# Optimization experiments

Hardware: AMD Instinct MI355X
Metric: run time of the kernel (lower is better)

## Reference

```python
import jax, jax.numpy as jnp
import numpy as np

K = 5  # Chebyshev order


def laplacian(w):
    # normalized Laplacian: I - D^{-1/2} W D^{-1/2}
    d = jnp.sum(w, axis=1)
    d_re = 1.0 / jnp.sqrt(d + 1e-5)
    return jnp.eye(w.shape[0], dtype=w.dtype) - d_re[:, None] * w * d_re[None, :]


def cheb_terms(x, lap, k):
    # x: [B,N,C], lap: [N,N] -> [B,k,N,C]
    # Faithful to torch code: T0 = ones, then (x, lap@x) recurrence for k>2.
    t0 = jnp.ones_like(x)
    if k == 1:
        return t0[:, None]
    t1 = jnp.matmul(lap, x)
    if k == 2:
        return jnp.stack([t0, t1], axis=1)
    terms = [t0, x, t1]
    tkm1, tk = x, t1
    for _ in range(3, k):
        tkm1, tk = tk, 2.0 * jnp.matmul(lap, tk) - tkm1
        terms.append(tk)
    return jnp.stack(terms, axis=1)


def graph_conv(x, lap, w, k):
    # torch: cp.permute(0,2,3,1).flatten(2) @ w, i.e. flat index = c*k + t
    t = cheb_terms(x, lap, k)                       # [B,k,N,C]
    C = x.shape[-1]
    O = w.shape[-1]
    return jnp.einsum('bknc,cko->bno', t, w.reshape(C, k, O))


def setup_inputs() -> dict:
    key = jax.random.key(0)
    ks = jax.random.split(key, 9)
    B, N, Cin, H = 8192, 32, 60, 128
    return {
        'x': jax.random.normal(ks[0], (B, N, Cin), dtype=jnp.float32),
        'adj': jax.random.normal(ks[1], (N, N), dtype=jnp.float32) * 0.1,
        'adj_bias': jax.random.normal(ks[2], (1,), dtype=jnp.float32) * 0.1 + 0.2,
        'w1': jax.random.normal(ks[3], (K * Cin, H), dtype=jnp.float32) * 0.05,
        'b1': jax.random.normal(ks[4], (1, 1, H), dtype=jnp.float32) * 0.05,
        'w2': jax.random.normal(ks[5], (K * H, H), dtype=jnp.float32) * 0.05,
        'b2': jax.random.normal(ks[6], (1, 1, H), dtype=jnp.float32) * 0.05,
        'fc_w': jax.random.normal(ks[7], (2, N * H), dtype=jnp.float32) * 0.02,
        'fc_b': jax.random.normal(ks[8], (2,), dtype=jnp.float32) * 0.02,
    }


def reference(x, adj, adj_bias, w1, b1, w2, b2, fc_w, fc_b):
    # DGCNN.forward (eval mode: dropout = identity)
    a = jax.nn.relu(adj + adj_bias)
    lap = laplacian(a)
    h = graph_conv(x, lap, w1, K)
    h = jax.nn.relu(h + b1)      # B1ReLU
    h = graph_conv(h, lap, w2, K)
    h = jax.nn.relu(h + b2)
    h = h.reshape(h.shape[0], -1)  # [B, N*H]
    return h @ fc_w.T + fc_b
```

## Files before the change

### kernel.cpp

```cpp
#include <hip/hip_runtime.h>

typedef unsigned short u16;
typedef unsigned int u32;
typedef short bf16x8 __attribute__((ext_vector_type(8)));
typedef float f32x4 __attribute__((ext_vector_type(4)));

#define MFMA16(a, b, c) __builtin_amdgcn_mfma_f32_16x16x32_bf16((a), (b), (c), 0, 0, 0)

__device__ __forceinline__ u16 f2bf(float f) {
  u32 u = __builtin_bit_cast(u32, f);
  u += 0x7FFFu + ((u >> 16) & 1u);
  return (u16)(u >> 16);
}
__device__ __forceinline__ u32 pk2bf(float a, float b) {
#if __has_builtin(__builtin_amdgcn_cvt_pk_bf16_f32)
  auto v = __builtin_amdgcn_cvt_pk_bf16_f32(a, b);
  return __builtin_bit_cast(u32, v);
#else
  return (u32)f2bf(a) | ((u32)f2bf(b) << 16);
#endif
}

#define WS_MGF   0
#define WS_WT1F  8192
#define WS_WT2F  73728
#define WS_B1    204800
#define WS_B2    205312

__global__ void prep_kernel(const float* __restrict__ adj,
                            const float* __restrict__ adj_bias,
                            const float* __restrict__ w1,
                            const float* __restrict__ b1,
                            const float* __restrict__ w2,
                            const float* __restrict__ b2,
                            char* __restrict__ ws) {
  const int tid = threadIdx.x;
  if (blockIdx.x == 0) {
    __shared__ float sa[1024], Ls[1024], L2s[1024], L3s[1024], sdre[32];
    float bias = adj_bias[0];
    for (int i = tid; i < 1024; i += 256) sa[i] = fmaxf(adj[i] + bias, 0.0f);
    __syncthreads();
    if (tid < 32) {
      float s = 0.0f;
      for (int c = 0; c < 32; ++c) s += sa[tid * 32 + c];
      sdre[tid] = 1.0f / sqrtf(s + 1e-5f);
    }
    __syncthreads();
    for (int i = tid; i < 1024; i += 256) {
      int n = i >> 5, c = i & 31;
      Ls[i] = (n == c ? 1.0f : 0.0f) - sdre[n] * sa[i] * sdre[c];
    }
    __syncthreads();
    for (int i = tid; i < 1024; i += 256) {
      int r = i >> 5, c = i & 31;
      float s = 0.0f;
      for (int m = 0; m < 32; ++m) s += Ls[r * 32 + m] * Ls[m * 32 + c];
      L2s[i] = s;
    }
    __syncthreads();
    for (int i = tid; i < 1024; i += 256) {
      int r = i >> 5, c = i & 31;
      float s = 0.0f;
      for (int m = 0; m < 32; ++m) s += L2s[r * 32 + m] * Ls[m * 32 + c];
      L3s[i] = s;
    }
    __syncthreads();
    u16* MGf = (u16*)(ws + WS_MGF);
    for (int i = tid; i < 4096; i += 256) {
      int jt = i >> 9, lane = (i >> 3) & 63, j = i & 7;
      int col = jt * 16 + (lane & 15);
      int k = ((lane >> 4) << 3) + j;
      int kk = col >> 5, np = col & 31;
      float v;
      if (kk == 0)      v = (np == k) ? 1.0f : 0.0f;
      else if (kk == 1) v = Ls[np * 32 + k];
      else if (kk == 2) v = 2.0f * L2s[np * 32 + k] - (np == k ? 1.0f : 0.0f);
      else              v = 4.0f * L3s[np * 32 + k] - 3.0f * Ls[np * 32 + k];
      MGf[i] = f2bf(v);
    }
    float* B1 = (float*)(ws + WS_B1);
    float* B2 = (float*)(ws + WS_B2);
    if (tid < 128) {
      float s = b1[tid];
      for (int c = 0; c < 60; ++c) s += w1[(c * 5) * 128 + tid];
      B1[tid] = s;
    } else {
      int o = tid - 128;
      float s = b2[o];
      for (int c = 0; c < 128; ++c) s += w2[(c * 5) * 128 + o];
      B2[o] = s;
    }
  } else {
    u16* WT1F = (u16*)(ws + WS_WT1F);
    u16* WT2F = (u16*)(ws + WS_WT2F);
    int g = (blockIdx.x - 1) * 256 + tid;
    for (int i = g; i < 32768; i += 16 * 256) {
      int j = i & 7, lane = (i >> 3) & 63, ks = (i >> 9) & 3;
      int h = (i >> 11) & 1, ot = i >> 12;
      int q = lane >> 4;
      int c = h * 32 + q * 8 + j;
      int o = ot * 16 + (lane & 15);
      WT1F[i] = (c < 60) ? f2bf(w1[(c * 5 + ks + 1) * 128 + o]) : (u16)0;
    }
    for (int i = g; i < 65536; i += 16 * 256) {
      int j = i & 7, lane = (i >> 3) & 63, ks = (i >> 9) & 3;
      int h = (i >> 11) & 3, mt = i >> 13;
      int q = lane >> 4;
      int c2 = h * 32 + q * 8 + j;
      int o = mt * 16 + (lane & 15);
      WT2F[i] = f2bf(w2[(c2 * 5 + ks + 1) * 128 + o]);
    }
  }
}

__global__ __launch_bounds__(256, 4) void dgcnn_kernel(
    const float* __restrict__ x,
    const char* __restrict__ ws,
    const float* __restrict__ fc_w,
    const float* __restrict__ fc_b,
    float* __restrict__ out) {
  __shared__ __align__(16) char arena[35840];
  __shared__ float red[16];
  u16* XtA = (u16*)arena;
  u16* XtB = (u16*)(arena + 5120);
  u16* HtA = (u16*)arena;
  u16* HtB = (u16*)(arena + 9216);
  u16* YA  = (u16*)(arena + 18432);
  u16* YB  = (u16*)(arena + 27136);

  const u16* MGf  = (const u16*)(ws + WS_MGF);
  const u16* WT1F = (const u16*)(ws + WS_WT1F);
  const u16* WT2F = (const u16*)(ws + WS_WT2F);
  const float* bias1 = (const float*)(ws + WS_B1);
  const float* bias2 = (const float*)(ws + WS_B2);

  const int tid = threadIdx.x;
  const int w = tid >> 6, lane = tid & 63;
  const int l15 = lane & 15, q = lane >> 4;
  const int b0 = blockIdx.x * 2;
  const f32x4 z4 = {0.0f, 0.0f, 0.0f, 0.0f};

  bf16x8 mB0 = *(const bf16x8*)(MGf + ((2 * w + 0) * 64 + lane) * 8);
  bf16x8 mB1 = *(const bf16x8*)(MGf + ((2 * w + 1) * 64 + lane) * 8);

  for (int i = tid; i < 160; i += 256) {
    int r = 60 + i / 40, c = i % 40;
    XtA[r * 40 + c] = 0;
    XtB[r * 40 + c] = 0;
  }
  const float* xb = x + (size_t)b0 * 1920;
  for (int i = tid; i < 1920; i += 256) {
    int n = i / 60, c = i - n * 60;
    u32 p = pk2bf(xb[i], xb[1920 + i]);
    XtA[c * 40 + n] = (u16)p;
    XtB[c * 40 + n] = (u16)(p >> 16);
  }
  __syncthreads();

  f32x4 acc1A[2][2] = {{z4, z4}, {z4, z4}};
  f32x4 acc1B[2][2] = {{z4, z4}, {z4, z4}};
#pragma unroll
  for (int h = 0; h < 2; ++h) {
    {
      f32x4 gA[2][2], gB[2][2];
#pragma unroll
      for (int mtl = 0; mtl < 2; ++mtl) {
        int roff = ((2 * h + mtl) * 16 + l15) * 40 + q * 8;
        bf16x8 aA = *(const bf16x8*)&XtA[roff];
        bf16x8 aB = *(const bf16x8*)&XtB[roff];
        gA[mtl][0] = MFMA16(aA, mB0, z4);
        gA[mtl][1] = MFMA16(aA, mB1, z4);
        gB[mtl][0] = MFMA16(aB, mB0, z4);
        gB[mtl][1] = MFMA16(aB, mB1, z4);
      }
#pragma unroll
      for (int mtl = 0; mtl < 2; ++mtl)
#pragma unroll
        for (int jtl = 0; jtl < 2; ++jtl) {
          int np = jtl * 16 + l15;
          int off = np * 136 + w * 32 + mtl * 16 + q * 4;
          uint2 vA, vB;
          vA.x = pk2bf(gA[mtl][jtl][0], gA[mtl][jtl][1]);
          vA.y = pk2bf(gA[mtl][jtl][2], gA[mtl][jtl][3]);
          vB.x = pk2bf(gB[mtl][jtl][0], gB[mtl][jtl][1]);
          vB.y = pk2bf(gB[mtl][jtl][2], gB[mtl][jtl][3]);
          *(uint2*)&YA[off] = vA;
          *(uint2*)&YB[off] = vB;
        }
    }
    __syncthreads();
#pragma unroll
    for (int ks = 0; ks < 4; ++ks) {
      bf16x8 wfa = *(const bf16x8*)(WT1F + ((((2 * w + 0) * 2 + h) * 4 + ks) * 64 + lane) * 8);
      bf16x8 wfb = *(const bf16x8*)(WT1F + ((((2 * w + 1) * 2 + h) * 4 + ks) * 64 + lane) * 8);
      int yoff = ks * 32 + q * 8;
      bf16x8 a0A = *(const bf16x8*)&YA[l15 * 136 + yoff];
      bf16x8 a1A = *(const bf16x8*)&YA[(16 + l15) * 136 + yoff];
      bf16x8 a0B = *(const bf16x8*)&YB[l15 * 136 + yoff];
      bf16x8 a1B = *(const bf16x8*)&YB[(16 + l15) * 136 + yoff];
      acc1A[0][0] = MFMA16(a0A, wfa, acc1A[0][0]);
      acc1A[0][1] = MFMA16(a0A, wfb, acc1A[0][1]);
      acc1A[1][0] = MFMA16(a1A, wfa, acc1A[1][0]);
      acc1A[1][1] = MFMA16(a1A, wfb, acc1A[1][1]);
      acc1B[0][0] = MFMA16(a0B, wfa, acc1B[0][0]);
      acc1B[0][1] = MFMA16(a0B, wfb, acc1B[0][1]);
      acc1B[1][0] = MFMA16(a1B, wfa, acc1B[1][0]);
      acc1B[1][1] = MFMA16(a1B, wfb, acc1B[1][1]);
    }
    if (h == 0) __syncthreads();
  }
#pragma unroll
  for (int ot = 0; ot < 2; ++ot) {
    int o = (2 * w + ot) * 16 + l15;
    float bv = bias1[o];
#pragma unroll
    for (int mt = 0; mt < 2; ++mt) {
      int off = o * 36 + mt * 16 + q * 4;
      uint2 vA, vB;
      vA.x = pk2bf(fmaxf(acc1A[mt][ot][0] + bv, 0.0f), fmaxf(acc1A[mt][ot][1] + bv, 0.0f));
      vA.y = pk2bf(fmaxf(acc1A[mt][ot][2] + bv, 0.0f), fmaxf(acc1A[mt][ot][3] + bv, 0.0f));
      vB.x = pk2bf(fmaxf(acc1B[mt][ot][0] + bv, 0.0f), fmaxf(acc1B[mt][ot][1] + bv, 0.0f));
      vB.y = pk2bf(fmaxf(acc1B[mt][ot][2] + bv, 0.0f), fmaxf(acc1B[mt][ot][3] + bv, 0.0f));
      *(uint2*)&HtA[off] = vA;
      *(uint2*)&HtB[off] = vB;
    }
  }
  __syncthreads();

  f32x4 acc2A[2][2] = {{z4, z4}, {z4, z4}};
  f32x4 acc2B[2][2] = {{z4, z4}, {z4, z4}};
#pragma unroll
  for (int h = 0; h < 4; ++h) {
    {
      f32x4 gA[2][2], gB[2][2];
#pragma unroll
      for (int mtl = 0; mtl < 2; ++mtl) {
        int roff = ((2 * h + mtl) * 16 + l15) * 36 + q * 8;
        bf16x8 aA = *(const bf16x8*)&HtA[roff];
        bf16x8 aB = *(const bf16x8*)&HtB[roff];
        gA[mtl][0] = MFMA16(aA, mB0, z4);
        gA[mtl][1] = MFMA16(aA, mB1, z4);
        gB[mtl][0] = MFMA16(aB, mB0, z4);
        gB[mtl][1] = MFMA16(aB, mB1, z4);
      }
#pragma unroll
      for (int mtl = 0; mtl < 2; ++mtl)
#pragma unroll
        for (int jtl = 0; jtl < 2; ++jtl) {
          int np = jtl * 16 + l15;
          int off = np * 136 + w * 32 + mtl * 16 + q * 4;
          uint2 vA, vB;
          vA.x = pk2bf(gA[mtl][jtl][0], gA[mtl][jtl][1]);
          vA.y = pk2bf(gA[mtl][jtl][2], gA[mtl][jtl][3]);
          vB.x = pk2bf(gB[mtl][jtl][0], gB[mtl][jtl][1]);
          vB.y = pk2bf(gB[mtl][jtl][2], gB[mtl][jtl][3]);
          *(uint2*)&YA[off] = vA;
          *(uint2*)&YB[off] = vB;
        }
    }
    __syncthreads();
#pragma unroll
    for (int ks = 0; ks < 4; ++ks) {
      bf16x8 wfa = *(const bf16x8*)(WT2F + ((((2 * w + 0) * 4 + h) * 4 + ks) * 64 + lane) * 8);
      bf16x8 wfb = *(const bf16x8*)(WT2F + ((((2 * w + 1) * 4 + h) * 4 + ks) * 64 + lane) * 8);
      int yoff = ks * 32 + q * 8;
      bf16x8 by0A = *(const bf16x8*)&YA[l15 * 136 + yoff];
      bf16x8 by1A = *(const bf16x8*)&YA[(16 + l15) * 136 + yoff];
      bf16x8 by0B = *(const bf16x8*)&YB[l15 * 136 + yoff];
      bf16x8 by1B = *(const bf16x8*)&YB[(16 + l15) * 136 + yoff];
      acc2A[0][0] = MFMA16(wfa, by0A, acc2A[0][0]);
      acc2A[0][1] = MFMA16(wfa, by1A, acc2A[0][1]);
      acc2A[1][0] = MFMA16(wfb, by0A, acc2A[1][0]);
      acc2A[1][1] = MFMA16(wfb, by1A, acc2A[1][1]);
      acc2B[0][0] = MFMA16(wfa, by0B, acc2B[0][0]);
      acc2B[0][1] = MFMA16(wfa, by1B, acc2B[0][1]);
      acc2B[1][0] = MFMA16(wfb, by0B, acc2B[1][0]);
      acc2B[1][1] = MFMA16(wfb, by1B, acc2B[1][1]);
    }
    if (h < 3) __syncthreads();
  }

  float p0A = 0.0f, p1A = 0.0f, p0B = 0.0f, p1B = 0.0f;
#pragma unroll
  for (int ot = 0; ot < 2; ++ot) {
    int ob = (2 * w + ot) * 16 + q * 4;
    float4 bv = *(const float4*)&bias2[ob];
#pragma unroll
    for (int nt = 0; nt < 2; ++nt) {
      int n = nt * 16 + l15;
      float4 w0 = *(const float4*)&fc_w[n * 128 + ob];
      float4 w1v = *(const float4*)&fc_w[4096 + n * 128 + ob];
      float hA0 = fmaxf(acc2A[ot][nt][0] + bv.x, 0.0f);
      float hA1 = fmaxf(acc2A[ot][nt][1] + bv.y, 0.0f);
      float hA2 = fmaxf(acc2A[ot][nt][2] + bv.z, 0.0f);
      float hA3 = fmaxf(acc2A[ot][nt][3] + bv.w, 0.0f);
      float hB0 = fmaxf(acc2B[ot][nt][0] + bv.x, 0.0f);
      float hB1 = fmaxf(acc2B[ot][nt][1] + bv.y, 0.0f);
      float hB2 = fmaxf(acc2B[ot][nt][2] + bv.z, 0.0f);
      float hB3 = fmaxf(acc2B[ot][nt][3] + bv.w, 0.0f);
      p0A = fmaf(hA0, w0.x, fmaf(hA1, w0.y, fmaf(hA2, w0.z, fmaf(hA3, w0.w, p0A))));
      p1A = fmaf(hA0, w1v.x, fmaf(hA1, w1v.y, fmaf(hA2, w1v.z, fmaf(hA3, w1v.w, p1A))));
      p0B = fmaf(hB0, w0.x, fmaf(hB1, w0.y, fmaf(hB2, w0.z, fmaf(hB3, w0.w, p0B))));
      p1B = fmaf(hB0, w1v.x, fmaf(hB1, w1v.y, fmaf(hB2, w1v.z, fmaf(hB3, w1v.w, p1B))));
    }
  }
#pragma unroll
  for (int off = 32; off >= 1; off >>= 1) {
    p0A += __shfl_xor(p0A, off);
    p1A += __shfl_xor(p1A, off);
    p0B += __shfl_xor(p0B, off);
    p1B += __shfl_xor(p1B, off);
  }
  if (lane == 0) {
    red[w * 4 + 0] = p0A;
    red[w * 4 + 1] = p1A;
    red[w * 4 + 2] = p0B;
    red[w * 4 + 3] = p1B;
  }
  __syncthreads();
  if (tid < 4) {
    float s = red[tid] + red[4 + tid] + red[8 + tid] + red[12 + tid] + fc_b[tid & 1];
    out[(b0 + (tid >> 1)) * 2 + (tid & 1)] = s;
  }
}

extern "C" void kernel_launch(void* const* d_in, const int* in_sizes, int n_in,
                              void* d_out, int out_size, void* d_ws, size_t ws_size,
                              hipStream_t stream) {
  const float* x        = (const float*)d_in[0];
  const float* adj      = (const float*)d_in[1];
  const float* adj_bias = (const float*)d_in[2];
  const float* w1       = (const float*)d_in[3];
  const float* b1       = (const float*)d_in[4];
  const float* w2       = (const float*)d_in[5];
  const float* b2       = (const float*)d_in[6];
  const float* fc_w     = (const float*)d_in[7];
  const float* fc_b     = (const float*)d_in[8];
  float* out = (float*)d_out;
  char* ws   = (char*)d_ws;

  prep_kernel<<<17, 256, 0, stream>>>(adj, adj_bias, w1, b1, w2, b2, ws);
  dgcnn_kernel<<<4096, 256, 0, stream>>>(x, ws, fc_w, fc_b, out);
}
```

Before: 194.7 us.

## Swizzle LDS layouts, vectorize input staging, shrink shared memory for higher occupancy

```diff
diff --git a/kernel.cpp b/kernel.cpp
--- a/kernel.cpp
+++ b/kernel.cpp
@@ -4,6 +4,7 @@
 typedef unsigned int u32;
 typedef short bf16x8 __attribute__((ext_vector_type(8)));
 typedef float f32x4 __attribute__((ext_vector_type(4)));
+typedef u32 u32x4 __attribute__((ext_vector_type(4)));
 
 #define MFMA16(a, b, c) __builtin_amdgcn_mfma_f32_16x16x32_bf16((a), (b), (c), 0, 0, 0)
 
@@ -98,7 +99,7 @@
       int j = i & 7, lane = (i >> 3) & 63, ks = (i >> 9) & 3;
       int h = (i >> 11) & 1, ot = i >> 12;
       int q = lane >> 4;
-      int c = h * 32 + q * 8 + j;
+      int c = h * 32 + ((j >> 2) << 4) + q * 4 + (j & 3);
       int o = ot * 16 + (lane & 15);
       WT1F[i] = (c < 60) ? f2bf(w1[(c * 5 + ks + 1) * 128 + o]) : (u16)0;
     }
@@ -106,27 +107,27 @@
       int j = i & 7, lane = (i >> 3) & 63, ks = (i >> 9) & 3;
       int h = (i >> 11) & 3, mt = i >> 13;
       int q = lane >> 4;
-      int c2 = h * 32 + q * 8 + j;
+      int c2 = h * 32 + ((j >> 2) << 4) + q * 4 + (j & 3);
       int o = mt * 16 + (lane & 15);
       WT2F[i] = f2bf(w2[(c2 * 5 + ks + 1) * 128 + o]);
     }
   }
 }
 
-__global__ __launch_bounds__(256, 4) void dgcnn_kernel(
+__global__ __launch_bounds__(256, 5) void dgcnn_kernel(
     const float* __restrict__ x,
     const char* __restrict__ ws,
     const float* __restrict__ fc_w,
     const float* __restrict__ fc_b,
     float* __restrict__ out) {
-  __shared__ __align__(16) char arena[35840];
-  __shared__ float red[16];
+  __shared__ __align__(16) char arena[32768];
   u16* XtA = (u16*)arena;
   u16* XtB = (u16*)(arena + 5120);
   u16* HtA = (u16*)arena;
-  u16* HtB = (u16*)(arena + 9216);
-  u16* YA  = (u16*)(arena + 18432);
-  u16* YB  = (u16*)(arena + 27136);
+  u16* HtB = (u16*)(arena + 8192);
+  u16* YA  = (u16*)(arena + 16384);
+  u16* YB  = (u16*)(arena + 24576);
+  float* red = (float*)arena;
 
   const u16* MGf  = (const u16*)(ws + WS_MGF);
   const u16* WT1F = (const u16*)(ws + WS_WT1F);
@@ -143,19 +144,34 @@
   bf16x8 mB0 = *(const bf16x8*)(MGf + ((2 * w + 0) * 64 + lane) * 8);
   bf16x8 mB1 = *(const bf16x8*)(MGf + ((2 * w + 1) * 64 + lane) * 8);
 
-  for (int i = tid; i < 160; i += 256) {
-    int r = 60 + i / 40, c = i % 40;
-    XtA[r * 40 + c] = 0;
-    XtB[r * 40 + c] = 0;
-  }
   const float* xb = x + (size_t)b0 * 1920;
-  for (int i = tid; i < 1920; i += 256) {
-    int n = i / 60, c = i - n * 60;
-    u32 p = pk2bf(xb[i], xb[1920 + i]);
-    XtA[c * 40 + n] = (u16)p;
-    XtB[c * 40 + n] = (u16)(p >> 16);
+  {
+    int tn = (tid & 15) * 2;
+    int tc = (tid >> 4) * 4;
+    if (tc < 60) {
+      float4 a0 = *(const float4*)(xb + tn * 60 + tc);
+      float4 a1 = *(const float4*)(xb + tn * 60 + 60 + tc);
+      float4 c0 = *(const float4*)(xb + 1920 + tn * 60 + tc);
+      float4 c1 = *(const float4*)(xb + 1920 + tn * 60 + 60 + tc);
+      *(u32*)&XtA[(tc + 0) * 40 + tn] = pk2bf(a0.x, a1.x);
+      *(u32*)&XtA[(tc + 1) * 40 + tn] = pk2bf(a0.y, a1.y);
+      *(u32*)&XtA[(tc + 2) * 40 + tn] = pk2bf(a0.z, a1.z);
+      *(u32*)&XtA[(tc + 3) * 40 + tn] = pk2bf(a0.w, a1.w);
+      *(u32*)&XtB[(tc + 0) * 40 + tn] = pk2bf(c0.x, c1.x);
+      *(u32*)&XtB[(tc + 1) * 40 + tn] = pk2bf(c0.y, c1.y);
+      *(u32*)&XtB[(tc + 2) * 40 + tn] = pk2bf(c0.z, c1.z);
+      *(u32*)&XtB[(tc + 3) * 40 + tn] = pk2bf(c0.w, c1.w);
+    } else {
+#pragma unroll
+      for (int j = 0; j < 4; ++j) {
+        *(u32*)&XtA[(tc + j) * 40 + tn] = 0;
+        *(u32*)&XtB[(tc + j) * 40 + tn] = 0;
+      }
+    }
   }
   __syncthreads();
+
+  const int ysw_w = ((w * 4 + q) ^ (l15 & 7)) * 8;
 
   f32x4 acc1A[2][2] = {{z4, z4}, {z4, z4}};
   f32x4 acc1B[2][2] = {{z4, z4}, {z4, z4}};
@@ -174,30 +190,31 @@
         gB[mtl][1] = MFMA16(aB, mB1, z4);
       }
 #pragma unroll
-      for (int mtl = 0; mtl < 2; ++mtl)
-#pragma unroll
-        for (int jtl = 0; jtl < 2; ++jtl) {
-          int np = jtl * 16 + l15;
-          int off = np * 136 + w * 32 + mtl * 16 + q * 4;
-          uint2 vA, vB;
-          vA.x = pk2bf(gA[mtl][jtl][0], gA[mtl][jtl][1]);
-          vA.y = pk2bf(gA[mtl][jtl][2], gA[mtl][jtl][3]);
-          vB.x = pk2bf(gB[mtl][jtl][0], gB[mtl][jtl][1]);
-          vB.y = pk2bf(gB[mtl][jtl][2], gB[mtl][jtl][3]);
-          *(uint2*)&YA[off] = vA;
-          *(uint2*)&YB[off] = vB;
-        }
+      for (int jtl = 0; jtl < 2; ++jtl) {
+        int yoff = (jtl * 16 + l15) * 128 + ysw_w;
+        u32x4 vA = {pk2bf(gA[0][jtl][0], gA[0][jtl][1]),
+                    pk2bf(gA[0][jtl][2], gA[0][jtl][3]),
+                    pk2bf(gA[1][jtl][0], gA[1][jtl][1]),
+                    pk2bf(gA[1][jtl][2], gA[1][jtl][3])};
+        u32x4 vB = {pk2bf(gB[0][jtl][0], gB[0][jtl][1]),
+                    pk2bf(gB[0][jtl][2], gB[0][jtl][3]),
+                    pk2bf(gB[1][jtl][0], gB[1][jtl][1]),
+                    pk2bf(gB[1][jtl][2], gB[1][jtl][3])};
+        *(u32x4*)&YA[yoff] = vA;
+        *(u32x4*)&YB[yoff] = vB;
+      }
     }
     __syncthreads();
 #pragma unroll
     for (int ks = 0; ks < 4; ++ks) {
-      bf16x8 wfa = *(const bf16x8*)(WT1F + ((((2 * w + 0) * 2 + h) * 4 + ks) * 64 + lane) * 8);
-      bf16x8 wfb = *(const bf16x8*)(WT1F + ((((2 * w + 1) * 2 + h) * 4 + ks) * 64 + lane) * 8);
-      int yoff = ks * 32 + q * 8;
-      bf16x8 a0A = *(const bf16x8*)&YA[l15 * 136 + yoff];
-      bf16x8 a1A = *(const bf16x8*)&YA[(16 + l15) * 136 + yoff];
-      bf16x8 a0B = *(const bf16x8*)&YB[l15 * 136 + yoff];
-      bf16x8 a1B = *(const bf16x8*)&YB[(16 + l15) * 136 + yoff];
+      const u16* wp = WT1F + (size_t)((((2 * w) * 2 + h) * 4 + ks) * 64 + lane) * 8;
+      bf16x8 wfa = *(const bf16x8*)wp;
+      bf16x8 wfb = *(const bf16x8*)(wp + 4096);
+      int ysw = ((ks * 4 + q) ^ (l15 & 7)) * 8;
+      bf16x8 a0A = *(const bf16x8*)&YA[l15 * 128 + ysw];
+      bf16x8 a1A = *(const bf16x8*)&YA[(16 + l15) * 128 + ysw];
+      bf16x8 a0B = *(const bf16x8*)&YB[l15 * 128 + ysw];
+      bf16x8 a1B = *(const bf16x8*)&YB[(16 + l15) * 128 + ysw];
       acc1A[0][0] = MFMA16(a0A, wfa, acc1A[0][0]);
       acc1A[0][1] = MFMA16(a0A, wfb, acc1A[0][1]);
       acc1A[1][0] = MFMA16(a1A, wfa, acc1A[1][0]);
@@ -215,14 +232,14 @@
     float bv = bias1[o];
 #pragma unroll
     for (int mt = 0; mt < 2; ++mt) {
-      int off = o * 36 + mt * 16 + q * 4;
+      int idx = o * 32 + (((mt * 2 + (q >> 1)) ^ (l15 & 3)) * 8) + (q & 1) * 4;
       uint2 vA, vB;
       vA.x = pk2bf(fmaxf(acc1A[mt][ot][0] + bv, 0.0f), fmaxf(acc1A[mt][ot][1] + bv, 0.0f));
       vA.y = pk2bf(fmaxf(acc1A[mt][ot][2] + bv, 0.0f), fmaxf(acc1A[mt][ot][3] + bv, 0.0f));
       vB.x = pk2bf(fmaxf(acc1B[mt][ot][0] + bv, 0.0f), fmaxf(acc1B[mt][ot][1] + bv, 0.0f));
       vB.y = pk2bf(fmaxf(acc1B[mt][ot][2] + bv, 0.0f), fmaxf(acc1B[mt][ot][3] + bv, 0.0f));
-      *(uint2*)&HtA[off] = vA;
-      *(uint2*)&HtB[off] = vB;
+      *(uint2*)&HtA[idx] = vA;
+      *(uint2*)&HtB[idx] = vB;
     }
   }
   __syncthreads();
@@ -235,7 +252,8 @@
       f32x4 gA[2][2], gB[2][2];
 #pragma unroll
       for (int mtl = 0; mtl < 2; ++mtl) {
-        int roff = ((2 * h + mtl) * 16 + l15) * 36 + q * 8;
+        int o2 = (2 * h + mtl) * 16 + l15;
+        int roff = o2 * 32 + ((q ^ (l15 & 3)) * 8);
         bf16x8 aA = *(const bf16x8*)&HtA[roff];
         bf16x8 aB = *(const bf16x8*)&HtB[roff];
         gA[mtl][0] = MFMA16(aA, mB0, z4);
@@ -244,30 +262,31 @@
         gB[mtl][1] = MFMA16(aB, mB1, z4);
       }
 #pragma unroll
-      for (int mtl = 0; mtl < 2; ++mtl)
-#pragma unroll
-        for (int jtl = 0; jtl < 2; ++jtl) {
-          int np = jtl * 16 + l15;
-          int off = np * 136 + w * 32 + mtl * 16 + q * 4;
-          uint2 vA, vB;
-          vA.x = pk2bf(gA[mtl][jtl][0], gA[mtl][jtl][1]);
-          vA.y = pk2bf(gA[mtl][jtl][2], gA[mtl][jtl][3]);
-          vB.x = pk2bf(gB[mtl][jtl][0], gB[mtl][jtl][1]);
-          vB.y = pk2bf(gB[mtl][jtl][2], gB[mtl][jtl][3]);
-          *(uint2*)&YA[off] = vA;
-          *(uint2*)&YB[off] = vB;
-        }
+      for (int jtl = 0; jtl < 2; ++jtl) {
+        int yoff = (jtl * 16 + l15) * 128 + ysw_w;
+        u32x4 vA = {pk2bf(gA[0][jtl][0], gA[0][jtl][1]),
+                    pk2bf(gA[0][jtl][2], gA[0][jtl][3]),
+                    pk2bf(gA[1][jtl][0], gA[1][jtl][1]),
+                    pk2bf(gA[1][jtl][2], gA[1][jtl][3])};
+        u32x4 vB = {pk2bf(gB[0][jtl][0], gB[0][jtl][1]),
+                    pk2bf(gB[0][jtl][2], gB[0][jtl][3]),
+                    pk2bf(gB[1][jtl][0], gB[1][jtl][1]),
+                    pk2bf(gB[1][jtl][2], gB[1][jtl][3])};
+        *(u32x4*)&YA[yoff] = vA;
+        *(u32x4*)&YB[yoff] = vB;
+      }
     }
     __syncthreads();
 #pragma unroll
     for (int ks = 0; ks < 4; ++ks) {
-      bf16x8 wfa = *(const bf16x8*)(WT2F + ((((2 * w + 0) * 4 + h) * 4 + ks) * 64 + lane) * 8);
-      bf16x8 wfb = *(const bf16x8*)(WT2F + ((((2 * w + 1) * 4 + h) * 4 + ks) * 64 + lane) * 8);
-      int yoff = ks * 32 + q * 8;
-      bf16x8 by0A = *(const bf16x8*)&YA[l15 * 136 + yoff];
-      bf16x8 by1A = *(const bf16x8*)&YA[(16 + l15) * 136 + yoff];
-      bf16x8 by0B = *(const bf16x8*)&YB[l15 * 136 + yoff];
-      bf16x8 by1B = *(const bf16x8*)&YB[(16 + l15) * 136 + yoff];
+      const u16* wp = WT2F + (size_t)((((2 * w) * 4 + h) * 4 + ks) * 64 + lane) * 8;
+      bf16x8 wfa = *(const bf16x8*)wp;
+      bf16x8 wfb = *(const bf16x8*)(wp + 8192);
+      int ysw = ((ks * 4 + q) ^ (l15 & 7)) * 8;
+      bf16x8 by0A = *(const bf16x8*)&YA[l15 * 128 + ysw];
+      bf16x8 by1A = *(const bf16x8*)&YA[(16 + l15) * 128 + ysw];
+      bf16x8 by0B = *(const bf16x8*)&YB[l15 * 128 + ysw];
+      bf16x8 by1B = *(const bf16x8*)&YB[(16 + l15) * 128 + ysw];
       acc2A[0][0] = MFMA16(wfa, by0A, acc2A[0][0]);
       acc2A[0][1] = MFMA16(wfa, by1A, acc2A[0][1]);
       acc2A[1][0] = MFMA16(wfb, by0A, acc2A[1][0]);
```

Result: faster. 185.4 us (-4.8%).

## Reorder graph conv to apply weights before Laplacian, dropping block-wide syncs

Applied to the files above, without the earlier changes.

```diff
diff --git a/kernel.cpp b/kernel.cpp
--- a/kernel.cpp
+++ b/kernel.cpp
@@ -4,6 +4,7 @@
 typedef unsigned int u32;
 typedef short bf16x8 __attribute__((ext_vector_type(8)));
 typedef float f32x4 __attribute__((ext_vector_type(4)));
+typedef u32 u32x4 __attribute__((ext_vector_type(4)));
 
 #define MFMA16(a, b, c) __builtin_amdgcn_mfma_f32_16x16x32_bf16((a), (b), (c), 0, 0, 0)
 
@@ -13,12 +14,9 @@
   return (u16)(u >> 16);
 }
 __device__ __forceinline__ u32 pk2bf(float a, float b) {
-#if __has_builtin(__builtin_amdgcn_cvt_pk_bf16_f32)
-  auto v = __builtin_amdgcn_cvt_pk_bf16_f32(a, b);
-  return __builtin_bit_cast(u32, v);
-#else
-  return (u32)f2bf(a) | ((u32)f2bf(b) << 16);
-#endif
+  u32 ua = __builtin_bit_cast(u32, a) + 0x8000u;
+  u32 ub = __builtin_bit_cast(u32, b) + 0x8000u;
+  return (ua >> 16) | (ub & 0xFFFF0000u);
 }
 
 #define WS_MGF   0
@@ -95,20 +93,20 @@
     u16* WT2F = (u16*)(ws + WS_WT2F);
     int g = (blockIdx.x - 1) * 256 + tid;
     for (int i = g; i < 32768; i += 16 * 256) {
-      int j = i & 7, lane = (i >> 3) & 63, ks = (i >> 9) & 3;
-      int h = (i >> 11) & 1, ot = i >> 12;
+      int j = i & 7, lane = (i >> 3) & 63, kt = (i >> 9) & 3;
+      int cs = (i >> 11) & 1, ot8 = i >> 12;
       int q = lane >> 4;
-      int c = h * 32 + q * 8 + j;
-      int o = ot * 16 + (lane & 15);
-      WT1F[i] = (c < 60) ? f2bf(w1[(c * 5 + ks + 1) * 128 + o]) : (u16)0;
+      int c = cs * 32 + q * 8 + j;
+      int o = ot8 * 16 + (lane & 15);
+      WT1F[i] = (c < 60) ? f2bf(w1[(c * 5 + kt + 1) * 128 + o]) : (u16)0;
     }
     for (int i = g; i < 65536; i += 16 * 256) {
-      int j = i & 7, lane = (i >> 3) & 63, ks = (i >> 9) & 3;
-      int h = (i >> 11) & 3, mt = i >> 13;
+      int j = i & 7, lane = (i >> 3) & 63, kt = (i >> 9) & 3;
+      int s = (i >> 11) & 3, ot8 = i >> 13;
       int q = lane >> 4;
-      int c2 = h * 32 + q * 8 + j;
-      int o = mt * 16 + (lane & 15);
-      WT2F[i] = f2bf(w2[(c2 * 5 + ks + 1) * 128 + o]);
+      int o1 = s * 32 + q * 8 + j;
+      int o2 = ot8 * 16 + (lane & 15);
+      WT2F[i] = f2bf(w2[(o1 * 5 + kt + 1) * 128 + o2]);
     }
   }
 }
@@ -119,14 +117,10 @@
     const float* __restrict__ fc_w,
     const float* __restrict__ fc_b,
     float* __restrict__ out) {
-  __shared__ __align__(16) char arena[35840];
-  __shared__ float red[16];
-  u16* XtA = (u16*)arena;
-  u16* XtB = (u16*)(arena + 5120);
-  u16* HtA = (u16*)arena;
-  u16* HtB = (u16*)(arena + 9216);
-  u16* YA  = (u16*)(arena + 18432);
-  u16* YB  = (u16*)(arena + 27136);
+  __shared__ __align__(16) char arena[33856];
+  u16* Hn = (u16*)arena;
+  u16* Zt = (u16*)(arena + 17408);
+  float* red = (float*)(arena + 33792);
 
   const u16* MGf  = (const u16*)(ws + WS_MGF);
   const u16* WT1F = (const u16*)(ws + WS_WT1F);
@@ -140,144 +134,135 @@
   const int b0 = blockIdx.x * 2;
   const f32x4 z4 = {0.0f, 0.0f, 0.0f, 0.0f};
 
-  bf16x8 mB0 = *(const bf16x8*)(MGf + ((2 * w + 0) * 64 + lane) * 8);
-  bf16x8 mB1 = *(const bf16x8*)(MGf + ((2 * w + 1) * 64 + lane) * 8);
-
-  for (int i = tid; i < 160; i += 256) {
-    int r = 60 + i / 40, c = i % 40;
-    XtA[r * 40 + c] = 0;
-    XtB[r * 40 + c] = 0;
-  }
-  const float* xb = x + (size_t)b0 * 1920;
-  for (int i = tid; i < 1920; i += 256) {
-    int n = i / 60, c = i - n * 60;
-    u32 p = pk2bf(xb[i], xb[1920 + i]);
-    XtA[c * 40 + n] = (u16)p;
-    XtB[c * 40 + n] = (u16)(p >> 16);
-  }
+  u16* zt0 = Zt + (w * 2 + 0) * 1024;
+  u16* zt1 = Zt + (w * 2 + 1) * 1024;
+
+  const int zswz = (l15 & 3) ^ (l15 >> 2);
+  int zws[2][2], zrd[2];
+#pragma unroll
+  for (int mtl = 0; mtl < 2; ++mtl)
+#pragma unroll
+    for (int ot = 0; ot < 2; ++ot)
+      zws[mtl][ot] = (ot * 16 + l15) * 32 + (((mtl * 2 + (q >> 1)) ^ zswz) * 8) + (q & 1) * 4;
+  zrd[0] = l15 * 32 + ((q ^ zswz) * 8);
+  zrd[1] = (16 + l15) * 32 + ((q ^ zswz) * 8);
+
+#define ZPACK(dst, t)                                        \
+  { uint2 v_;                                                \
+    v_.x = pk2bf((t)[0], (t)[1]);                            \
+    v_.y = pk2bf((t)[2], (t)[3]);                            \
+    *(uint2*)&(dst) = v_; }
+
+  f32x4 acc1[2][2][2];
+#pragma unroll
+  for (int a = 0; a < 2; ++a)
+#pragma unroll
+    for (int b = 0; b < 2; ++b)
+#pragma unroll
+      for (int c = 0; c < 2; ++c) acc1[a][b][c] = z4;
+
+#pragma unroll
+  for (int bat = 0; bat < 2; ++bat) {
+    u16* z = bat ? zt1 : zt0;
+    bf16x8 xf[2][2];
+#pragma unroll
+    for (int mtl = 0; mtl < 2; ++mtl)
+#pragma unroll
+      for (int cs = 0; cs < 2; ++cs) {
+        int n = mtl * 16 + l15, c0 = cs * 32 + q * 8;
+        const float* p = x + (size_t)(b0 + bat) * 1920 + n * 60 + c0;
+        float4 u = *(const float4*)p;
+        float4 v = (c0 < 56) ? *(const float4*)(p + 4)
+                             : make_float4(0.0f, 0.0f, 0.0f, 0.0f);
+        u32x4 pk = {pk2bf(u.x, u.y), pk2bf(u.z, u.w), pk2bf(v.x, v.y), pk2bf(v.z, v.w)};
+        xf[mtl][cs] = __builtin_bit_cast(bf16x8, pk);
+      }
+#pragma unroll
+    for (int kt = 0; kt < 4; ++kt) {
+      bf16x8 m0 = *(const bf16x8*)(MGf + (kt * 2 + 0) * 512 + lane * 8);
+      bf16x8 m1 = *(const bf16x8*)(MGf + (kt * 2 + 1) * 512 + lane * 8);
+      const u16* wp = WT1F + (size_t)((2 * w) * 8 + kt) * 512 + lane * 8;
+      bf16x8 wf00 = *(const bf16x8*)wp;
+      bf16x8 wf01 = *(const bf16x8*)(wp + 2048);
+      bf16x8 wf10 = *(const bf16x8*)(wp + 4096);
+      bf16x8 wf11 = *(const bf16x8*)(wp + 6144);
+      f32x4 zc00 = MFMA16(xf[0][0], wf00, z4); zc00 = MFMA16(xf[0][1], wf01, zc00);
+      f32x4 zc01 = MFMA16(xf[0][0], wf10, z4); zc01 = MFMA16(xf[0][1], wf11, zc01);
+      f32x4 zc10 = MFMA16(xf[1][0], wf00, z4); zc10 = MFMA16(xf[1][1], wf01, zc10);
+      f32x4 zc11 = MFMA16(xf[1][0], wf10, z4); zc11 = MFMA16(xf[1][1], wf11, zc11);
+      ZPACK(z[zws[0][0]], zc00);
+      ZPACK(z[zws[0][1]], zc01);
+      ZPACK(z[zws[1][0]], zc10);
+      ZPACK(z[zws[1][1]], zc11);
+      bf16x8 za0 = *(const bf16x8*)&z[zrd[0]];
+      bf16x8 za1 = *(const bf16x8*)&z[zrd[1]];
+      acc1[bat][0][0] = MFMA16(za0, m0, acc1[bat][0][0]);
+      acc1[bat][0][1] = MFMA16(za0, m1, acc1[bat][0][1]);
+      acc1[bat][1][0] = MFMA16(za1, m0, acc1[bat][1][0]);
+      acc1[bat][1][1] = MFMA16(za1, m1, acc1[bat][1][1]);
+    }
+  }
+
+#pragma unroll
+  for (int bat = 0; bat < 2; ++bat)
+#pragma unroll
+    for (int otl = 0; otl < 2; ++otl) {
+      int ob = (2 * w + otl) * 16 + q * 4;
+      float4 bv = *(const float4*)&bias1[ob];
+#pragma unroll
+      for (int npt = 0; npt < 2; ++npt) {
+        f32x4 a = acc1[bat][otl][npt];
+        uint2 v;
+        v.x = pk2bf(fmaxf(a[0] + bv.x, 0.0f), fmaxf(a[1] + bv.y, 0.0f));
+        v.y = pk2bf(fmaxf(a[2] + bv.z, 0.0f), fmaxf(a[3] + bv.w, 0.0f));
+        *(uint2*)&Hn[bat * 4352 + (npt * 16 + l15) * 136 + ob] = v;
+      }
+    }
   __syncthreads();
 
-  f32x4 acc1A[2][2] = {{z4, z4}, {z4, z4}};
-  f32x4 acc1B[2][2] = {{z4, z4}, {z4, z4}};
-#pragma unroll
-  for (int h = 0; h < 2; ++h) {
-    {
-      f32x4 gA[2][2], gB[2][2];
-#pragma unroll
-      for (int mtl = 0; mtl < 2; ++mtl) {
-        int roff = ((2 * h + mtl) * 16 + l15) * 40 + q * 8;
-        bf16x8 aA = *(const bf16x8*)&XtA[roff];
-        bf16x8 aB = *(const bf16x8*)&XtB[roff];
-        gA[mtl][0] = MFMA16(aA, mB0, z4);
-        gA[mtl][1] = MFMA16(aA, mB1, z4);
-        gB[mtl][0] = MFMA16(aB, mB0, z4);
-        gB[mtl][1] = MFMA16(aB, mB1, z4);
+  f32x4 acc2[2][2][2];
+#pragma unroll
+  for (int a = 0; a < 2; ++a)
+#pragma unroll
+    for (int b = 0; b < 2; ++b)
+#pragma unroll
+      for (int c = 0; c < 2; ++c) acc2[a][b][c] = z4;
+
+#pragma unroll
+  for (int bat = 0; bat < 2; ++bat) {
+    u16* z = bat ? zt1 : zt0;
+    bf16x8 hf[2][4];
+#pragma unroll
+    for (int ntl = 0; ntl < 2; ++ntl)
+#pragma unroll
+      for (int s = 0; s < 4; ++s)
+        hf[ntl][s] = *(const bf16x8*)&Hn[bat * 4352 + (ntl * 16 + l15) * 136 + s * 32 + q * 8];
+#pragma unroll
+    for (int kt = 0; kt < 4; ++kt) {
+      bf16x8 m0 = *(const bf16x8*)(MGf + (kt * 2 + 0) * 512 + lane * 8);
+      bf16x8 m1 = *(const bf16x8*)(MGf + (kt * 2 + 1) * 512 + lane * 8);
+      f32x4 zc00 = z4, zc01 = z4, zc10 = z4, zc11 = z4;
+#pragma unroll
+      for (int s = 0; s < 4; ++s) {
+        const u16* wp = WT2F + (size_t)((2 * w) * 16 + s * 4 + kt) * 512 + lane * 8;
+        bf16x8 w0  = *(const bf16x8*)wp;
+        bf16x8 w1f = *(const bf16x8*)(wp + 8192);
+        zc00 = MFMA16(hf[0][s], w0, zc00);
+        zc01 = MFMA16(hf[0][s], w1f, zc01);
+        zc10 = MFMA16(hf[1][s], w0, zc10);
+        zc11 = MFMA16(hf[1][s], w1f, zc11);
       }
-#pragma unroll
-      for (int mtl = 0; mtl < 2; ++mtl)
-#pragma unroll
-        for (int jtl = 0; jtl < 2; ++jtl) {
-          int np = jtl * 16 + l15;
-          int off = np * 136 + w * 32 + mtl * 16 + q * 4;
-          uint2 vA, vB;
-          vA.x = pk2bf(gA[mtl][jtl][0], gA[mtl][jtl][1]);
-          vA.y = pk2bf(gA[mtl][jtl][2], gA[mtl][jtl][3]);
-          vB.x = pk2bf(gB[mtl][jtl][0], gB[mtl][jtl][1]);
-          vB.y = pk2bf(gB[mtl][jtl][2], gB[mtl][jtl][3]);
-          *(uint2*)&YA[off] = vA;
-          *(uint2*)&YB[off] = vB;
-        }
-    }
-    __syncthreads();
-#pragma unroll
-    for (int ks = 0; ks < 4; ++ks) {
-      bf16x8 wfa = *(const bf16x8*)(WT1F + ((((2 * w + 0) * 2 + h) * 4 + ks) * 64 + lane) * 8);
-      bf16x8 wfb = *(const bf16x8*)(WT1F + ((((2 * w + 1) * 2 + h) * 4 + ks) * 64 + lane) * 8);
-      int yoff = ks * 32 + q * 8;
-      bf16x8 a0A = *(const bf16x8*)&YA[l15 * 136 + yoff];
-      bf16x8 a1A = *(const bf16x8*)&YA[(16 + l15) * 136 + yoff];
-      bf16x8 a0B = *(const bf16x8*)&YB[l15 * 136 + yoff];
-      bf16x8 a1B = *(const bf16x8*)&YB[(16 + l15) * 136 + yoff];
-      acc1A[0][0] = MFMA16(a0A, wfa, acc1A[0][0]);
-      acc1A[0][1] = MFMA16(a0A, wfb, acc1A[0][1]);
-      acc1A[1][0] = MFMA16(a1A, wfa, acc1A[1][0]);
-      acc1A[1][1] = MFMA16(a1A, wfb, acc1A[1][1]);
-      acc1B[0][0] = MFMA16(a0B, wfa, acc1B[0][0]);
-      acc1B[0][1] = MFMA16(a0B, wfb, acc1B[0][1]);
-      acc1B[1][0] = MFMA16(a1B, wfa, acc1B[1][0]);
-      acc1B[1][1] = MFMA16(a1B, wfb, acc1B[1][1]);
-    }
-    if (h == 0) __syncthreads();
-  }
-#pragma unroll
-  for (int ot = 0; ot < 2; ++ot) {
-    int o = (2 * w + ot) * 16 + l15;
-    float bv = bias1[o];
-#pragma unroll
-    for (int mt = 0; mt < 2; ++mt) {
-      int off = o * 36 + mt * 16 + q * 4;
-      uint2 vA, vB;
-      vA.x = pk2bf(fmaxf(acc1A[mt][ot][0] + bv, 0.0f), fmaxf(acc1A[mt][ot][1] + bv, 0.0f));
-      vA.y = pk2bf(fmaxf(acc1A[mt][ot][2] + bv, 0.0f), fmaxf(acc1A[mt][ot][3] + bv, 0.0f));
-      vB.x = pk2bf(fmaxf(acc1B[mt][ot][0] + bv, 0.0f), fmaxf(acc1B[mt][ot][1] + bv, 0.0f));
-      vB.y = pk2bf(fmaxf(acc1B[mt][ot][2] + bv, 0.0f), fmaxf(acc1B[mt][ot][3] + bv, 0.0f));
-      *(uint2*)&HtA[off] = vA;
-      *(uint2*)&HtB[off] = vB;
-    }
-  }
-  __syncthreads();
-
-  f32x4 acc2A[2][2] = {{z4, z4}, {z4, z4}};
-  f32x4 acc2B[2][2] = {{z4, z4}, {z4, z4}};
-#pragma unroll
-  for (int h = 0; h < 4; ++h) {
-    {
-      f32x4 gA[2][2], gB[2][2];
-#pragma unroll
-      for (int mtl = 0; mtl < 2; ++mtl) {
-        int roff = ((2 * h + mtl) * 16 + l15) * 36 + q * 8;
-        bf16x8 aA = *(const bf16x8*)&HtA[roff];
-        bf16x8 aB = *(const bf16x8*)&HtB[roff];
-        gA[mtl][0] = MFMA16(aA, mB0, z4);
-        gA[mtl][1] = MFMA16(aA, mB1, z4);
-        gB[mtl][0] = MFMA16(aB, mB0, z4);
-        gB[mtl][1] = MFMA16(aB, mB1, z4);
-      }
-#pragma unroll
-      for (int mtl = 0; mtl < 2; ++mtl)
-#pragma unroll
-        for (int jtl = 0; jtl < 2; ++jtl) {
-          int np = jtl * 16 + l15;
-          int off = np * 136 + w * 32 + mtl * 16 + q * 4;
-          uint2 vA, vB;
-          vA.x = pk2bf(gA[mtl][jtl][0], gA[mtl][jtl][1]);
-          vA.y = pk2bf(gA[mtl][jtl][2], gA[mtl][jtl][3]);
-          vB.x = pk2bf(gB[mtl][jtl][0], gB[mtl][jtl][1]);
-          vB.y = pk2bf(gB[mtl][jtl][2], gB[mtl][jtl][3]);
-          *(uint2*)&YA[off] = vA;
-          *(uint2*)&YB[off] = vB;
-        }
-    }
-    __syncthreads();
-#pragma unroll
-    for (int ks = 0; ks < 4; ++ks) {
-      bf16x8 wfa = *(const bf16x8*)(WT2F + ((((2 * w + 0) * 4 + h) * 4 + ks) * 64 + lane) * 8);
-      bf16x8 wfb = *(const bf16x8*)(WT2F + ((((2 * w + 1) * 4 + h) * 4 + ks) * 64 + lane) * 8);
-      int yoff = ks * 32 + q * 8;
-      bf16x8 by0A = *(const bf16x8*)&YA[l15 * 136 + yoff];
-      bf16x8 by1A = *(const bf16x8*)&YA[(16 + l15) * 136 + yoff];
-      bf16x8 by0B = *(const bf16x8*)&YB[l15 * 136 + yoff];
-      bf16x8 by1B = *(const bf16x8*)&YB[(16 + l15) * 136 + yoff];
-      acc2A[0][0] = MFMA16(wfa, by0A, acc2A[0][0]);
-      acc2A[0][1] = MFMA16(wfa, by1A, acc2A[0][1]);
-      acc2A[1][0] = MFMA16(wfb, by0A, acc2A[1][0]);
-      acc2A[1][1] = MFMA16(wfb, by1A, acc2A[1][1]);
-      acc2B[0][0] = MFMA16(wfa, by0B, acc2B[0][0]);
-      acc2B[0][1] = MFMA16(wfa, by1B, acc2B[0][1]);
-      acc2B[1][0] = MFMA16(wfb, by0B, acc2B[1][0]);
-      acc2B[1][1] = MFMA16(wfb, by1B, acc2B[1][1]);
-    }
-    if (h < 3) __syncthreads();
+      ZPACK(z[zws[0][0]], zc00);
+      ZPACK(z[zws[0][1]], zc01);
+      ZPACK(z[zws[1][0]], zc10);
+      ZPACK(z[zws[1][1]], zc11);
+      bf16x8 za0 = *(const bf16x8*)&z[zrd[0]];
+      bf16x8 za1 = *(const bf16x8*)&z[zrd[1]];
+      acc2[bat][0][0] = MFMA16(za0, m0, acc2[bat][0][0]);
+      acc2[bat][0][1] = MFMA16(za0, m1, acc2[bat][0][1]);
+      acc2[bat][1][0] = MFMA16(za1, m0, acc2[bat][1][0]);
+      acc2[bat][1][1] = MFMA16(za1, m1, acc2[bat][1][1]);
+    }
   }
 
   float p0A = 0.0f, p1A = 0.0f, p0B = 0.0f, p1B = 0.0f;
@@ -290,14 +275,14 @@
       int n = nt * 16 + l15;
       float4 w0 = *(const float4*)&fc_w[n * 128 + ob];
       float4 w1v = *(const float4*)&fc_w[4096 + n * 128 + ob];
-      float hA0 = fmaxf(acc2A[ot][nt][0] + bv.x, 0.0f);
-      float hA1 = fmaxf(acc2A[ot][nt][1] + bv.y, 0.0f);
-      float hA2 = fmaxf(acc2A[ot][nt][2] + bv.z, 0.0f);
-      float hA3 = fmaxf(acc2A[ot][nt][3] + bv.w, 0.0f);
-      float hB0 = fmaxf(acc2B[ot][nt][0] + bv.x, 0.0f);
-      float hB1 = fmaxf(acc2B[ot][nt][1] + bv.y, 0.0f);
-      float hB2 = fmaxf(acc2B[ot][nt][2] + bv.z, 0.0f);
-      float hB3 = fmaxf(acc2B[ot][nt][3] + bv.w, 0.0f);
+      float hA0 = fmaxf(acc2[0][ot][nt][0] + bv.x, 0.0f);
+      float hA1 = fmaxf(acc2[0][ot][nt][1] + bv.y, 0.0f);
+      float hA2 = fmaxf(acc2[0][ot][nt][2] + bv.z, 0.0f);
+      float hA3 = fmaxf(acc2[0][ot][nt][3] + bv.w, 0.0f);
+      float hB0 = fmaxf(acc2[1][ot][nt][0] + bv.x, 0.0f);
+      float hB1 = fmaxf(acc2[1][ot][nt][1] + bv.y, 0.0f);
+      float hB2 = fmaxf(acc2[1][ot][nt][2] + bv.z, 0.0f);
+      float hB3 = fmaxf(acc2[1][ot][nt][3] + bv.w, 0.0f);
       p0A = fmaf(hA0, w0.x, fmaf(hA1, w0.y, fmaf(hA2, w0.z, fmaf(hA3, w0.w, p0A))));
       p1A = fmaf(hA0, w1v.x, fmaf(hA1, w1v.y, fmaf(hA2, w1v.z, fmaf(hA3, w1v.w, p1A))));
       p0B = fmaf(hB0, w0.x, fmaf(hB1, w0.y, fmaf(hB2, w0.z, fmaf(hB3, w0.w, p0B))));
```

Result: no change. 197.7 us (+1.6%).
